# Kernel optimization log

Hardware: AMD Instinct MI355X
Metric: run time of the kernel (lower is better)

Reference implementation:

```python
import jax, jax.numpy as jnp
import numpy as np

B, N, D_IN, D, H_HEADS, DH, M_LAND, ITERS, NCLS = 2, 16384, 1024, 512, 8, 64, 256, 6, 2


def layer_norm(x, g, b, eps=1e-5):
    mu = x.mean(-1, keepdims=True)
    var = ((x - mu) ** 2).mean(-1, keepdims=True)
    return (x - mu) * jax.lax.rsqrt(var + eps) * g + b


def pinv_iter(x, iters):
    # Moore-Penrose pseudo-inverse via Newton-Schulz style iteration (lucidrains nystrom-attention)
    col = jnp.abs(x).sum(-1)
    row = jnp.abs(x).sum(-2)
    z = jnp.swapaxes(x, -1, -2) / (jnp.max(col) * jnp.max(row))
    I = jnp.eye(x.shape[-1], dtype=x.dtype)
    for _ in range(iters):
        xz = x @ z
        z = 0.25 * z @ (13.0 * I - xz @ (15.0 * I - xz @ (7.0 * I - xz)))
    return z


def depthwise_conv(x, w, pad_h, pad_w):
    # x: [B,C,H,W], w: [C,1,kh,kw], groups=C
    return jax.lax.conv_general_dilated(
        x, w, (1, 1), ((pad_h, pad_h), (pad_w, pad_w)),
        dimension_numbers=('NCHW', 'OIHW', 'NCHW'), feature_group_count=x.shape[1])


def nystrom_attention(x, w_qkv, w_out, b_out, res_w):
    b, n, _ = x.shape
    pad = (-n) % M_LAND
    xp = jnp.pad(x, ((0, 0), (pad, 0), (0, 0)))  # pad at front
    npad = n + pad
    qkv = xp @ w_qkv                              # [b, npad, 3D]
    q, k, v = jnp.split(qkv, 3, axis=-1)
    split_heads = lambda t: t.reshape(b, npad, H_HEADS, DH).transpose(0, 2, 1, 3)
    q = split_heads(q) * (DH ** -0.5)
    k = split_heads(k)
    v = split_heads(v)
    l = npad // M_LAND
    # landmarks: mean over contiguous groups '(m l) d -> m d'
    ql = q.reshape(b, H_HEADS, M_LAND, l, DH).mean(3)
    kl = k.reshape(b, H_HEADS, M_LAND, l, DH).mean(3)
    sim1 = jnp.einsum('bhnd,bhmd->bhnm', q, kl)   # [b,h,npad,m]
    sim2 = jnp.einsum('bhid,bhjd->bhij', ql, kl)  # [b,h,m,m]
    sim3 = jnp.einsum('bhmd,bhnd->bhmn', ql, k)   # [b,h,m,npad]
    a1 = jax.nn.softmax(sim1, -1)
    a2 = jax.nn.softmax(sim2, -1)
    a3 = jax.nn.softmax(sim3, -1)
    a2inv = pinv_iter(a2, ITERS)
    out = (a1 @ a2inv) @ (a3 @ v)                 # [b,h,npad,dh]
    # residual depthwise conv over sequence dim, kernel (33,1), per head
    out = out + depthwise_conv(v, res_w, 16, 0)
    out = out.transpose(0, 2, 1, 3).reshape(b, npad, D)
    out = out @ w_out + b_out                     # dropout is identity in eval
    return out[:, -n:]


def ppeg(x, Hs, Ws, w7, b7, w5, b5, w3, b3):
    Bx, _, C = x.shape
    cls_tok, feat = x[:, :1], x[:, 1:]
    f = feat.transpose(0, 2, 1).reshape(Bx, C, Hs, Ws)
    y = (f
         + depthwise_conv(f, w7, 3, 3) + b7[None, :, None, None]
         + depthwise_conv(f, w5, 2, 2) + b5[None, :, None, None]
         + depthwise_conv(f, w3, 1, 1) + b3[None, :, None, None])
    y = y.reshape(Bx, C, Hs * Ws).transpose(0, 2, 1)
    return jnp.concatenate([cls_tok, y], axis=1)


def _forward(x, w_feat, b_feat, cls_token, ln1_g, ln1_b, qkv1, out1_w, out1_b, res1_w,
             ppeg_w7, ppeg_b7, ppeg_w5, ppeg_b5, ppeg_w3, ppeg_b3,
             ln2_g, ln2_b, qkv2, out2_w, out2_b, res2_w, lnf_g, lnf_b, cls_w, cls_b):
    h = jax.nn.gelu(x @ w_feat + b_feat)          # feature embed (dropout off)
    n = h.shape[1]
    side = int(np.ceil(np.sqrt(n)))
    add = side * side - n
    h = jnp.concatenate([h, h[:, :add]], axis=1)  # pad bag to square
    cls = jnp.broadcast_to(cls_token, (h.shape[0], 1, D))
    h = jnp.concatenate([cls, h], axis=1)
    h = h + nystrom_attention(layer_norm(h, ln1_g, ln1_b), qkv1, out1_w, out1_b, res1_w)
    h = ppeg(h, side, side, ppeg_w7, ppeg_b7, ppeg_w5, ppeg_b5, ppeg_w3, ppeg_b3)
    h = h + nystrom_attention(layer_norm(h, ln2_g, ln2_b), qkv2, out2_w, out2_b, res2_w)
    feat0 = layer_norm(h, lnf_g, lnf_b)[:, 0]
    return feat0 @ cls_w + cls_b                  # logits [B, n_classes]


def setup_inputs() -> dict:
    key = jax.random.key(0)
    ks = jax.random.split(key, 16)
    s = jnp.float32(0.02)
    return {
        'x': jax.random.normal(ks[0], (B, N, D_IN), jnp.float32),
        'w_feat': jax.random.normal(ks[1], (D_IN, D), jnp.float32) * s,
        'b_feat': jnp.zeros((D,), jnp.float32),
        'cls_token': jax.random.normal(ks[2], (1, 1, D), jnp.float32) * jnp.float32(1e-6),
        'ln1_g': jnp.ones((D,), jnp.float32), 'ln1_b': jnp.zeros((D,), jnp.float32),
        'qkv1': jax.random.normal(ks[3], (D, 3 * D), jnp.float32) * s,
        'out1_w': jax.random.normal(ks[4], (D, D), jnp.float32) * s,
        'out1_b': jnp.zeros((D,), jnp.float32),
        'res1_w': jax.random.normal(ks[5], (H_HEADS, 1, 33, 1), jnp.float32) * s,
        'ppeg_w7': jax.random.normal(ks[6], (D, 1, 7, 7), jnp.float32) * s,
        'ppeg_b7': jnp.zeros((D,), jnp.float32),
        'ppeg_w5': jax.random.normal(ks[7], (D, 1, 5, 5), jnp.float32) * s,
        'ppeg_b5': jnp.zeros((D,), jnp.float32),
        'ppeg_w3': jax.random.normal(ks[8], (D, 1, 3, 3), jnp.float32) * s,
        'ppeg_b3': jnp.zeros((D,), jnp.float32),
        'ln2_g': jnp.ones((D,), jnp.float32), 'ln2_b': jnp.zeros((D,), jnp.float32),
        'qkv2': jax.random.normal(ks[9], (D, 3 * D), jnp.float32) * s,
        'out2_w': jax.random.normal(ks[10], (D, D), jnp.float32) * s,
        'out2_b': jnp.zeros((D,), jnp.float32),
        'res2_w': jax.random.normal(ks[11], (H_HEADS, 1, 33, 1), jnp.float32) * s,
        'lnf_g': jnp.ones((D,), jnp.float32), 'lnf_b': jnp.zeros((D,), jnp.float32),
        'cls_w': jax.random.normal(ks[12], (D, NCLS), jnp.float32) * s,
        'cls_b': jnp.zeros((NCLS,), jnp.float32),
    }


def reference(x, w_feat, b_feat, cls_token, ln1_g, ln1_b, qkv1, out1_w, out1_b, res1_w,
              ppeg_w7, ppeg_b7, ppeg_w5, ppeg_b5, ppeg_w3, ppeg_b3,
              ln2_g, ln2_b, qkv2, out2_w, out2_b, res2_w, lnf_g, lnf_b, cls_w, cls_b):
    return _forward(x, w_feat, b_feat, cls_token, ln1_g, ln1_b, qkv1, out1_w, out1_b, res1_w,
                    ppeg_w7, ppeg_b7, ppeg_w5, ppeg_b5, ppeg_w3, ppeg_b3,
                    ln2_g, ln2_b, qkv2, out2_w, out2_b, res2_w, lnf_g, lnf_b, cls_w, cls_b)
```

## Files before the change

kernel.cpp:

```cpp
#include <hip/hip_runtime.h>
#include <cstdint>
#include <cstddef>

#define BB 2
#define TT 16385
#define NPAD 16640
#define DD 512
#define HH 8
#define DHH 64
#define MLAND 256
#define PADF 255
#define A3KC 26
#define A3CH 640

typedef __attribute__((ext_vector_type(8))) _Float16 f16x8;
typedef __attribute__((ext_vector_type(4))) float f32x4;

__device__ __forceinline__ float gelu_f(float v) {
  float c = 0.7978845608028654f * (v + 0.044715f * v * v * v);
  return 0.5f * v * (1.0f + tanhf(c));
}

__device__ __forceinline__ unsigned short f16_1(float a) {
  _Float16 h = (_Float16)a;
  return __builtin_bit_cast(unsigned short, h);
}
__device__ __forceinline__ float f16f(unsigned u) {
  return (float)__builtin_bit_cast(_Float16, (unsigned short)(u & 0xffffu));
}
__device__ __forceinline__ unsigned pk_f16(float a, float b) {
  return (unsigned)f16_1(a) | ((unsigned)f16_1(b) << 16);
}
__device__ __forceinline__ void split2h(float a, float b, unsigned& hi, unsigned& lo) {
  _Float16 ah = (_Float16)a, bh = (_Float16)b;
  hi = (unsigned)__builtin_bit_cast(unsigned short, ah) |
       ((unsigned)__builtin_bit_cast(unsigned short, bh) << 16);
  lo = pk_f16(a - (float)ah, b - (float)bh);
}
__device__ __forceinline__ void store4h(float4 v, unsigned short* dh,
                                        unsigned short* dl) {
  unsigned h0, l0, h1, l1;
  split2h(v.x, v.y, h0, l0);
  split2h(v.z, v.w, h1, l1);
  *(uint2*)dh = make_uint2(h0, h1);
  *(uint2*)dl = make_uint2(l0, l1);
}

__device__ __forceinline__ void gload16(const unsigned short* g, short* l) {
  __builtin_amdgcn_global_load_lds(
      (const __attribute__((address_space(1))) void*)g,
      (__attribute__((address_space(3))) void*)l, 16, 0, 0);
}

__global__ void k_set_cls(float* __restrict__ h, const float* __restrict__ cls) {
  h[(size_t)blockIdx.x * TT * DD + threadIdx.x] = cls[threadIdx.x];
}
__global__ void k_copy_cls(float* __restrict__ dst, const float* __restrict__ src) {
  size_t o = (size_t)blockIdx.x * TT * DD + threadIdx.x;
  dst[o] = src[o];
}

__global__ __launch_bounds__(256) void k_cvt_wt(
    const float* __restrict__ W, unsigned short* __restrict__ Wth, int K, int N) {
  __shared__ float tile[32][33];
  int kb = blockIdx.x * 32, nb = blockIdx.y * 32;
  int t = threadIdx.x;
  int tr = t >> 3, tc4 = (t & 7) * 4;
  float4 v = *(const float4*)(W + (size_t)(kb + tr) * N + nb + tc4);
  tile[tr][tc4 + 0] = v.x;
  tile[tr][tc4 + 1] = v.y;
  tile[tr][tc4 + 2] = v.z;
  tile[tr][tc4 + 3] = v.w;
  __syncthreads();
  int n = nb + tr;
  ushort4 hs;
  hs.x = f16_1(tile[tc4 + 0][tr]);
  hs.y = f16_1(tile[tc4 + 1][tr]);
  hs.z = f16_1(tile[tc4 + 2][tr]);
  hs.w = f16_1(tile[tc4 + 3][tr]);
  *(ushort4*)(Wth + (size_t)n * K + kb + tc4) = hs;
}

template <int MODE>
__global__ __launch_bounds__(512) void k_gemm_mfma(
    const float* __restrict__ A, const unsigned short* __restrict__ Aph,
    const unsigned short* __restrict__ Apl, const unsigned short* __restrict__ Wth,
    const float* __restrict__ bias, void* __restrict__ Cv, int M, int K, int N,
    int lda) {
  __shared__ short Ash[128][44];
  __shared__ short Asl[128][44];
  __shared__ short Bsh[256][44];
  const int t = threadIdx.x;
  int nRow = gridDim.x, nCol = gridDim.y;
  int lin = blockIdx.x + blockIdx.y * nRow;
  int chunk = 8 * nCol;
  int group = lin / chunk;
  int rem = lin - group * chunk;
  int gbase = group * 8;
  int Geff = nRow - gbase;
  if (Geff > 8) Geff = 8;
  const int rb = (gbase + rem % Geff) * 128;
  const int cb = (rem / Geff) * 256;
  const float* Ab = A;
  float* Cf = (float*)Cv;
  unsigned short* Ch = (unsigned short*)Cv;
  if (MODE == 2) {
    int b = blockIdx.z;
    Ab = A + (size_t)b * NPAD * DD + (size_t)PADF * DD;
    Cf = (float*)Cv + (size_t)b * TT * DD;
  }
  const int lane = t & 63, wv = t >> 6;
  const int wr = wv >> 2, wc = wv & 3;
  const int fr = lane & 15, kg = lane >> 4;
  const int srow = t >> 2, skh = (t & 3) * 8;
  const int brow = t >> 1, bkh = (t & 1) * 16;

  f32x4 acc[4][4];
  f32x4 zero4 = {0.f, 0.f, 0.f, 0.f};
#pragma unroll
  for (int i = 0; i < 4; ++i)
#pragma unroll
    for (int j = 0; j < 4; ++j) acc[i][j] = zero4;

  for (int k0 = 0; k0 < K; k0 += 32) {
    __syncthreads();
    if (MODE == 1) {
      const unsigned short* ph = Aph + (size_t)(rb + srow) * lda + k0 + skh;
      const unsigned short* pl = Apl + (size_t)(rb + srow) * lda + k0 + skh;
      *(uint4*)&Ash[srow][skh] = *(const uint4*)ph;
      *(uint4*)&Asl[srow][skh] = *(const uint4*)pl;
    } else {
      int grow = rb + srow;
      float4 f0 = {0, 0, 0, 0}, f1 = {0, 0, 0, 0};
      if (grow < M) {
        const float* p = Ab + (size_t)grow * lda + k0 + skh;
        f0 = *(const float4*)p;
        f1 = *(const float4*)(p + 4);
      }
      unsigned h0, h1, h2, h3, l0, l1, l2, l3;
      split2h(f0.x, f0.y, h0, l0);
      split2h(f0.z, f0.w, h1, l1);
      split2h(f1.x, f1.y, h2, l2);
      split2h(f1.z, f1.w, h3, l3);
      *(uint4*)&Ash[srow][skh] = make_uint4(h0, h1, h2, h3);
      *(uint4*)&Asl[srow][skh] = make_uint4(l0, l1, l2, l3);
    }
    {
      const unsigned short* ph = Wth + (size_t)(cb + brow) * K + k0 + bkh;
      *(uint4*)&Bsh[brow][bkh] = *(const uint4*)ph;
      *(uint4*)&Bsh[brow][bkh + 8] = *(const uint4*)(ph + 8);
    }
    __syncthreads();
    f16x8 ah[4], al[4];
#pragma unroll
    for (int mf = 0; mf < 4; ++mf) {
      ah[mf] = *(const f16x8*)&Ash[wr * 64 + mf * 16 + fr][kg * 8];
      al[mf] = *(const f16x8*)&Asl[wr * 64 + mf * 16 + fr][kg * 8];
    }
#pragma unroll
    for (int nf = 0; nf < 4; ++nf) {
      f16x8 bhf = *(const f16x8*)&Bsh[wc * 64 + nf * 16 + fr][kg * 8];
#pragma unroll
      for (int mf = 0; mf < 4; ++mf) {
        acc[mf][nf] =
            __builtin_amdgcn_mfma_f32_16x16x32_f16(ah[mf], bhf, acc[mf][nf], 0, 0, 0);
        acc[mf][nf] =
            __builtin_amdgcn_mfma_f32_16x16x32_f16(al[mf], bhf, acc[mf][nf], 0, 0, 0);
      }
    }
  }
#pragma unroll
  for (int mf = 0; mf < 4; ++mf) {
#pragma unroll
    for (int r = 0; r < 4; ++r) {
      int row = rb + wr * 64 + mf * 16 + kg * 4 + r;
      if (MODE == 2 && row >= M) continue;
      size_t orow = (MODE == 0) ? (size_t)(row + (row >> 14) + 1) : (size_t)row;
#pragma unroll
      for (int nf = 0; nf < 4; ++nf) {
        int col = cb + wc * 64 + nf * 16 + fr;
        float v = acc[mf][nf][r];
        if (MODE == 0) {
          Cf[orow * DD + col] = gelu_f(v + bias[col]);
        } else if (MODE == 1) {
          Ch[orow * (size_t)N + col] = f16_1(v);
        } else {
          float old = Cf[orow * DD + col];
          Cf[orow * DD + col] = old + v + bias[col];
        }
      }
    }
  }
}

__global__ __launch_bounds__(512) void k_gemm_qkv8(
    const unsigned short* __restrict__ Aph, const unsigned short* __restrict__ Apl,
    const unsigned short* __restrict__ Wth, unsigned short* __restrict__ Ch) {
  __shared__ __align__(16) short Ah[2][128][32];
  __shared__ __align__(16) short Al[2][128][32];
  __shared__ __align__(16) short Bs[2][256][32];
  const int t = threadIdx.x;
  int nRow = gridDim.x, nCol = gridDim.y;
  int lin = blockIdx.x + blockIdx.y * nRow;
  int chunk = 8 * nCol;
  int group = lin / chunk;
  int rem = lin - group * chunk;
  int gbase = group * 8;
  int Geff = nRow - gbase;
  if (Geff > 8) Geff = 8;
  const int rb = (gbase + rem % Geff) * 128;
  const int cb = (rem / Geff) * 256;
  const int lane = t & 63, wv = t >> 6;
  const int wr = wv >> 2, wc = wv & 3;
  const int fr = lane & 15, kg = lane >> 4;
  const int lr4 = lane >> 2;
  const int ss = (lane & 3) ^ (lr4 & 3);

  f32x4 acc[4][4];
  f32x4 zero4 = {0.f, 0.f, 0.f, 0.f};
#pragma unroll
  for (int i = 0; i < 4; ++i)
#pragma unroll
    for (int j = 0; j < 4; ++j) acc[i][j] = zero4;

  auto STAGE = [&](int kt, int bf) {
    const int k0 = kt * 32;
    {
      int lr = wv * 16;
      gload16(Aph + (size_t)(rb + lr + lr4) * DD + k0 + ss * 8, &Ah[bf][lr][0]);
      gload16(Apl + (size_t)(rb + lr + lr4) * DD + k0 + ss * 8, &Al[bf][lr][0]);
    }
#pragma unroll
    for (int j = 0; j < 2; ++j) {
      int lr = wv * 32 + j * 16;
      gload16(Wth + (size_t)(cb + lr + lr4) * DD + k0 + ss * 8, &Bs[bf][lr][0]);
    }
  };

  STAGE(0, 0);
  STAGE(1, 1);
  const int sl = ((kg ^ (fr & 3))) * 8;
  for (int kt = 0; kt < 16; ++kt) {
    if (kt < 15) {
      asm volatile("s_waitcnt vmcnt(4)" ::: "memory");
    } else {
      asm volatile("s_waitcnt vmcnt(0)" ::: "memory");
    }
    __builtin_amdgcn_sched_barrier(0);
    __builtin_amdgcn_s_barrier();
    const int bf = kt & 1;
    f16x8 ah[4], al[4];
#pragma unroll
    for (int mf = 0; mf < 4; ++mf) {
      ah[mf] = *(const f16x8*)&Ah[bf][wr * 64 + mf * 16 + fr][sl];
      al[mf] = *(const f16x8*)&Al[bf][wr * 64 + mf * 16 + fr][sl];
    }
#pragma unroll
    for (int nf = 0; nf < 4; ++nf) {
      f16x8 bhf = *(const f16x8*)&Bs[bf][wc * 64 + nf * 16 + fr][sl];
#pragma unroll
      for (int mf = 0; mf < 4; ++mf) {
        acc[mf][nf] =
            __builtin_amdgcn_mfma_f32_16x16x32_f16(ah[mf], bhf, acc[mf][nf], 0, 0, 0);
        acc[mf][nf] =
            __builtin_amdgcn_mfma_f32_16x16x32_f16(al[mf], bhf, acc[mf][nf], 0, 0, 0);
      }
    }
    __builtin_amdgcn_s_barrier();
    if (kt + 2 < 16) STAGE(kt + 2, bf);
  }
#pragma unroll
  for (int mf = 0; mf < 4; ++mf) {
#pragma unroll
    for (int r = 0; r < 4; ++r) {
      int row = rb + wr * 64 + mf * 16 + kg * 4 + r;
#pragma unroll
      for (int nf = 0; nf < 4; ++nf) {
        int col = cb + wc * 64 + nf * 16 + fr;
        Ch[(size_t)row * 1536 + col] = f16_1(acc[mf][nf][r]);
      }
    }
  }
}

__global__ __launch_bounds__(256) void k_ln_pad(
    unsigned short* __restrict__ xph, unsigned short* __restrict__ xpl,
    const float* __restrict__ h, const float* __restrict__ gam,
    const float* __restrict__ bet) {
  int w = threadIdx.x >> 6, lane = threadIdx.x & 63;
  int row = blockIdx.x * 4 + w;
  if (row >= BB * TT) return;
  int b = row / TT, i = row - b * TT;
  const float* src = h + (size_t)row * DD;
  float4 x0 = *(const float4*)(src + lane * 4);
  float4 x1 = *(const float4*)(src + 256 + lane * 4);
  float s = x0.x + x0.y + x0.z + x0.w + x1.x + x1.y + x1.z + x1.w;
  for (int o = 32; o; o >>= 1) s += __shfl_xor(s, o);
  float mu = s * (1.f / 512.f);
  float q = (x0.x - mu) * (x0.x - mu) + (x0.y - mu) * (x0.y - mu) +
            (x0.z - mu) * (x0.z - mu) + (x0.w - mu) * (x0.w - mu) +
            (x1.x - mu) * (x1.x - mu) + (x1.y - mu) * (x1.y - mu) +
            (x1.z - mu) * (x1.z - mu) + (x1.w - mu) * (x1.w - mu);
  for (int o = 32; o; o >>= 1) q += __shfl_xor(q, o);
  float rs = rsqrtf(q * (1.f / 512.f) + 1e-5f);
  float4 g0 = *(const float4*)(gam + lane * 4);
  float4 g1 = *(const float4*)(gam + 256 + lane * 4);
  float4 b0 = *(const float4*)(bet + lane * 4);
  float4 b1 = *(const float4*)(bet + 256 + lane * 4);
  float4 o0, o1;
  o0.x = (x0.x - mu) * rs * g0.x + b0.x;
  o0.y = (x0.y - mu) * rs * g0.y + b0.y;
  o0.z = (x0.z - mu) * rs * g0.z + b0.z;
  o0.w = (x0.w - mu) * rs * g0.w + b0.w;
  o1.x = (x1.x - mu) * rs * g1.x + b1.x;
  o1.y = (x1.y - mu) * rs * g1.y + b1.y;
  o1.z = (x1.z - mu) * rs * g1.z + b1.z;
  o1.w = (x1.w - mu) * rs * g1.w + b1.w;
  size_t ro = ((size_t)b * NPAD + PADF + i) * DD;
  store4h(o0, xph + ro + lane * 4, xpl + ro + lane * 4);
  store4h(o1, xph + ro + 256 + lane * 4, xpl + ro + 256 + lane * 4);
}

__global__ void k_zero_pad(unsigned short* __restrict__ xph,
                           unsigned short* __restrict__ xpl) {
  int r = blockIdx.x;
  int b = r / PADF, j = r - b * PADF;
  size_t ro = ((size_t)b * NPAD + j) * DD;
  ((unsigned*)(xph + ro))[threadIdx.x] = 0u;
  ((unsigned*)(xpl + ro))[threadIdx.x] = 0u;
}

__global__ __launch_bounds__(256) void k_landmarks(
    float* __restrict__ ql, float* __restrict__ kl,
    const unsigned short* __restrict__ qkv) {
  int t = threadIdx.x;
  int mi = t >> 6, d = t & 63;
  int blk = blockIdx.x;
  int bh = blk >> 6, mg = blk & 63;
  int b = bh >> 3, h = bh & 7;
  int m = mg * 4 + mi;
  const unsigned short* base = qkv + (size_t)b * NPAD * 1536 + h * 64 + d;
  float sq = 0.f, sk = 0.f;
  int t0 = m * 65;
  for (int j = 0; j < 65; ++j) {
    const unsigned short* p = base + (size_t)(t0 + j) * 1536;
    sq += f16f(p[0]);
    sk += f16f(p[512]);
  }
  ql[((size_t)bh * 256 + m) * 64 + d] = sq * (0.125f / 65.f);
  kl[((size_t)bh * 256 + m) * 64 + d] = sk * (1.f / 65.f);
}

__global__ __launch_bounds__(256) void k_sim2(
    float* __restrict__ sim, const float* __restrict__ ql, const float* __restrict__ kl) {
  __shared__ __align__(16) float Aq[64][68];
  __shared__ __align__(16) float Bk[64][68];
  int t = threadIdx.x;
  int tj = blockIdx.x, ti = blockIdx.y, bh = blockIdx.z;
  int r = t >> 2, cc = (t & 3) * 16;
  const float* ap = ql + ((size_t)bh * 256 + ti * 64 + r) * 64 + cc;
  const float* bp = kl + ((size_t)bh * 256 + tj * 64 + r) * 64 + cc;
#pragma unroll
  for (int i = 0; i < 16; i += 4) {
    *(float4*)&Aq[r][cc + i] = *(const float4*)(ap + i);
    *(float4*)&Bk[r][cc + i] = *(const float4*)(bp + i);
  }
  __syncthreads();
  int tx = t & 15, ty = t >> 4;
  float acc[4][4];
#pragma unroll
  for (int i = 0; i < 4; ++i)
#pragma unroll
    for (int j = 0; j < 4; ++j) acc[i][j] = 0.f;
  for (int d = 0; d < 64; d += 4) {
    float4 a4[4], b4[4];
#pragma unroll
    for (int ii = 0; ii < 4; ++ii) a4[ii] = *(float4*)&Aq[ty * 4 + ii][d];
#pragma unroll
    for (int jj = 0; jj < 4; ++jj) b4[jj] = *(float4*)&Bk[tx * 4 + jj][d];
#pragma unroll
    for (int ii = 0; ii < 4; ++ii)
#pragma unroll
      for (int jj = 0; jj < 4; ++jj)
        acc[ii][jj] += a4[ii].x * b4[jj].x + a4[ii].y * b4[jj].y + a4[ii].z * b4[jj].z +
                       a4[ii].w * b4[jj].w;
  }
#pragma unroll
  for (int ii = 0; ii < 4; ++ii)
#pragma unroll
    for (int jj = 0; jj < 4; ++jj)
      sim[((size_t)bh * 256 + ti * 64 + ty * 4 + ii) * 256 + tj * 64 + tx * 4 + jj] =
          acc[ii][jj];
}

__global__ __launch_bounds__(256) void k_softmax256(float* __restrict__ a) {
  int w = threadIdx.x >> 6, lane = threadIdx.x & 63;
  size_t row = (size_t)blockIdx.x * 4 + w;
  float* p = a + row * 256 + lane * 4;
  float4 v = *(float4*)p;
  float m = fmaxf(fmaxf(v.x, v.y), fmaxf(v.z, v.w));
  for (int o = 32; o; o >>= 1) m = fmaxf(m, __shfl_xor(m, o));
  v.x = expf(v.x - m); v.y = expf(v.y - m);
  v.z = expf(v.z - m); v.w = expf(v.w - m);
  float s = v.x + v.y + v.z + v.w;
  for (int o = 32; o; o >>= 1) s += __shfl_xor(s, o);
  float inv = 1.f / s;
  v.x *= inv; v.y *= inv; v.z *= inv; v.w *= inv;
  *(float4*)p = v;
}

__global__ void k_pinv_sums(float* __restrict__ red, const float* __restrict__ a2) {
  int bh = blockIdx.x, t = threadIdx.x;
  const float* Ab = a2 + (size_t)bh * 65536;
  float s = 0.f;
  for (int i = 0; i < 256; ++i) s += fabsf(Ab[(size_t)i * 256 + t]);
  red[bh * 256 + t] = s;
  float c = 0.f;
  const float* rp = Ab + (size_t)t * 256;
  for (int j = 0; j < 256; j += 4) {
    float4 v = *(const float4*)(rp + j);
    c += fabsf(v.x) + fabsf(v.y) + fabsf(v.z) + fabsf(v.w);
  }
  red[4096 + bh * 256 + t] = c;
}

__global__ void k_pinv_scale(float* __restrict__ red) {
  __shared__ float sm[8];
  int t = threadIdx.x;
  float m1 = 0.f, m2 = 0.f;
  for (int k = t; k < 4096; k += 256) {
    m1 = fmaxf(m1, red[k]);
    m2 = fmaxf(m2, red[4096 + k]);
  }
  for (int o = 32; o; o >>= 1) {
    m1 = fmaxf(m1, __shfl_xor(m1, o));
    m2 = fmaxf(m2, __shfl_xor(m2, o));
  }
  int w = t >> 6;
  if ((t & 63) == 0) { sm[w] = m1; sm[4 + w] = m2; }
  __syncthreads();
  if (t == 0) {
    float a = fmaxf(fmaxf(sm[0], sm[1]), fmaxf(sm[2], sm[3]));
    float b = fmaxf(fmaxf(sm[4], sm[5]), fmaxf(sm[6], sm[7]));
    red[8192] = 1.0f / (a * b);
  }
}

__global__ void k_zinit(float* __restrict__ z, const float* __restrict__ a2,
                        const float* __restrict__ red) {
  float s = red[8192];
  int i = blockIdx.x, bh = blockIdx.y, j = threadIdx.x;
  z[((size_t)bh * 256 + i) * 256 + j] = a2[((size_t)bh * 256 + j) * 256 + i] * s;
}

__device__ __forceinline__ void bmm_core(
    short (*Ash)[136], short (*Asl)[136], short (*Bsh)[136], short (*Bsl)[136],
    const float* __restrict__ Ab, const float* __restrict__ Bb, int i0, int j0, int N,
    int t, f32x4 (&acc)[4]) {
  const int lane = t & 63, w = t >> 6;
  const int fr = lane & 15, kg = lane >> 4;
  const int ar = t >> 2, akseg = (t & 3) * 32;
  for (int k0 = 0; k0 < 256; k0 += 128) {
    __syncthreads();
    {
      const float* p = Ab + (size_t)(i0 + ar) * 256 + k0 + akseg;
#pragma unroll
      for (int q = 0; q < 4; ++q) {
        float4 f0 = *(const float4*)(p + q * 8);
        float4 f1 = *(const float4*)(p + q * 8 + 4);
        unsigned h0, h1, h2, h3, l0, l1, l2, l3;
        split2h(f0.x, f0.y, h0, l0);
        split2h(f0.z, f0.w, h1, l1);
        split2h(f1.x, f1.y, h2, l2);
        split2h(f1.z, f1.w, h3, l3);
        *(uint4*)&Ash[ar][akseg + q * 8] = make_uint4(h0, h1, h2, h3);
        *(uint4*)&Asl[ar][akseg + q * 8] = make_uint4(l0, l1, l2, l3);
      }
    }
    {
#pragma unroll
      for (int pass = 0; pass < 8; ++pass) {
        int kr = pass * 16 + (t >> 4);
        int jseg = (t & 15) * 4;
        const float* p = Bb + (size_t)(k0 + kr) * N + j0 + jseg;
        float4 f = *(const float4*)p;
        float fv[4] = {f.x, f.y, f.z, f.w};
#pragma unroll
        for (int c = 0; c < 4; ++c) {
          _Float16 hh = (_Float16)fv[c];
          float lo = fv[c] - (float)hh;
          Bsh[jseg + c][kr] = (short)__builtin_bit_cast(unsigned short, hh);
          Bsl[jseg + c][kr] = (short)f16_1(lo);
        }
      }
    }
    __syncthreads();
#pragma unroll
    for (int kw = 0; kw < 4; ++kw) {
      f16x8 bhf = *(const f16x8*)&Bsh[w * 16 + fr][kw * 32 + kg * 8];
      f16x8 blf = *(const f16x8*)&Bsl[w * 16 + fr][kw * 32 + kg * 8];
#pragma unroll
      for (int mf = 0; mf < 4; ++mf) {
        f16x8 ah = *(const f16x8*)&Ash[mf * 16 + fr][kw * 32 + kg * 8];
        f16x8 al = *(const f16x8*)&Asl[mf * 16 + fr][kw * 32 + kg * 8];
        acc[mf] = __builtin_amdgcn_mfma_f32_16x16x32_f16(ah, bhf, acc[mf], 0, 0, 0);
        acc[mf] = __builtin_amdgcn_mfma_f32_16x16x32_f16(al, bhf, acc[mf], 0, 0, 0);
        acc[mf] = __builtin_amdgcn_mfma_f32_16x16x32_f16(ah, blf, acc[mf], 0, 0, 0);
      }
    }
  }
}

__global__ __launch_bounds__(256) void k_bmm_poly(
    const float* __restrict__ A, const float* __restrict__ Bm,
    const float* __restrict__ E, float* __restrict__ C, float a1, float d1, float e1,
    int N) {
  __shared__ short Ash[64][136];
  __shared__ short Asl[64][136];
  __shared__ short Bsh[64][136];
  __shared__ short Bsl[64][136];
  const int t = threadIdx.x;
  const int bh = blockIdx.z;
  const int i0 = blockIdx.y * 64, j0 = blockIdx.x * 64;
  const int lane = t & 63, w = t >> 6;
  const int fr = lane & 15, kg = lane >> 4;
  f32x4 acc[4];
  f32x4 zero4 = {0.f, 0.f, 0.f, 0.f};
#pragma unroll
  for (int i = 0; i < 4; ++i) acc[i] = zero4;
  bmm_core(Ash, Asl, Bsh, Bsl, A + (size_t)bh * 65536, Bm + (size_t)bh * 256 * N, i0,
           j0, N, t, acc);
  int j = j0 + w * 16 + fr;
#pragma unroll
  for (int mf = 0; mf < 4; ++mf) {
#pragma unroll
    for (int rr = 0; rr < 4; ++rr) {
      int i = i0 + mf * 16 + kg * 4 + rr;
      float v = acc[mf][rr];
      size_t off = (size_t)bh * 256 * N + (size_t)i * N + j;
      float out = a1 * v + ((i == j) ? d1 : 0.f);
      if (E) out += e1 * E[off];
      C[off] = out;
    }
  }
}

__global__ __launch_bounds__(256) void k_bmm_dual(
    const float* __restrict__ A0, const float* __restrict__ A1,
    const float* __restrict__ Bm, float* __restrict__ C0, float* __restrict__ C1,
    float s) {
  __shared__ short Ash[64][136];
  __shared__ short Asl[64][136];
  __shared__ short Bsh[64][136];
  __shared__ short Bsl[64][136];
  const int t = threadIdx.x;
  const int z = blockIdx.z;
  const int bh = z & 15;
  const int sel = z >> 4;
  const float* A = sel ? A1 : A0;
  float* C = sel ? C1 : C0;
  const int i0 = blockIdx.y * 64, j0 = blockIdx.x * 64;
  const int lane = t & 63, w = t >> 6;
  const int fr = lane & 15, kg = lane >> 4;
  f32x4 acc[4];
  f32x4 zero4 = {0.f, 0.f, 0.f, 0.f};
#pragma unroll
  for (int i = 0; i < 4; ++i) acc[i] = zero4;
  bmm_core(Ash, Asl, Bsh, Bsl, A + (size_t)bh * 65536, Bm + (size_t)bh * 65536, i0, j0,
           256, t, acc);
  int j = j0 + w * 16 + fr;
#pragma unroll
  for (int mf = 0; mf < 4; ++mf) {
#pragma unroll
    for (int rr = 0; rr < 4; ++rr) {
      int i = i0 + mf * 16 + kg * 4 + rr;
      size_t off = (size_t)bh * 65536 + (size_t)i * 256 + j;
      C[off] = s * acc[mf][rr];
    }
  }
}

__global__ __launch_bounds__(256, 2) void k_a3v_mfma(
    float* __restrict__ pacc, float* __restrict__ pL,
    const float* __restrict__ ql, const unsigned short* __restrict__ qkv) {
  __shared__ short Ks[64][72];
  __shared__ short Vt[64][72];
  __shared__ short Ps[4][64][72];
  const int t = threadIdx.x;
  const int bh = blockIdx.x;
  const int kc = blockIdx.y;
  const int b = bh >> 3, h = bh & 7;
  const int lane = t & 63, w = t >> 6;
  const int fr = lane & 15, kg = lane >> 4;

  f16x8 qf[4][2];
#pragma unroll
  for (int nf = 0; nf < 4; ++nf) {
    const float* qp = ql + ((size_t)bh * 256 + w * 64 + nf * 16 + fr) * 64 + kg * 8;
#pragma unroll
    for (int kw = 0; kw < 2; ++kw) {
      float4 a = *(const float4*)(qp + kw * 32);
      float4 c = *(const float4*)(qp + kw * 32 + 4);
      uint4 uu = make_uint4(pk_f16(a.x, a.y), pk_f16(a.z, a.w), pk_f16(c.x, c.y),
                            pk_f16(c.z, c.w));
      qf[nf][kw] = *(f16x8*)&uu;
    }
  }
  f32x4 oacc[4][4];
  f32x4 zero4 = {0.f, 0.f, 0.f, 0.f};
#pragma unroll
  for (int i = 0; i < 4; ++i)
#pragma unroll
    for (int j = 0; j < 4; ++j) oacc[i][j] = zero4;
  float Lp[4] = {0.f, 0.f, 0.f, 0.f};

  const int skey = t >> 2, sd = (t & 3) * 16;
  const unsigned short* kbase = qkv + (size_t)b * NPAD * 1536 + 512 + h * 64 + sd;

  for (int it = 0; it < A3CH / 64; ++it) {
    int nt = kc * A3CH + it * 64;
    __syncthreads();
    {
      const unsigned short* kp = kbase + (size_t)(nt + skey) * 1536;
      *(uint4*)&Ks[skey][sd] = *(const uint4*)kp;
      *(uint4*)&Ks[skey][sd + 8] = *(const uint4*)(kp + 8);
      const unsigned short* vp = kp + 512;
      uint4 v01 = *(const uint4*)vp;
      uint4 v23 = *(const uint4*)(vp + 8);
      Vt[sd + 0][skey] = (short)v01.x;
      Vt[sd + 1][skey] = (short)(v01.x >> 16);
      Vt[sd + 2][skey] = (short)v01.y;
      Vt[sd + 3][skey] = (short)(v01.y >> 16);
      Vt[sd + 4][skey] = (short)v01.z;
      Vt[sd + 5][skey] = (short)(v01.z >> 16);
      Vt[sd + 6][skey] = (short)v01.w;
      Vt[sd + 7][skey] = (short)(v01.w >> 16);
      Vt[sd + 8][skey] = (short)v23.x;
      Vt[sd + 9][skey] = (short)(v23.x >> 16);
      Vt[sd + 10][skey] = (short)v23.y;
      Vt[sd + 11][skey] = (short)(v23.y >> 16);
      Vt[sd + 12][skey] = (short)v23.z;
      Vt[sd + 13][skey] = (short)(v23.z >> 16);
      Vt[sd + 14][skey] = (short)v23.w;
      Vt[sd + 15][skey] = (short)(v23.w >> 16);
    }
    __syncthreads();
    f32x4 sacc[4][4];
#pragma unroll
    for (int i = 0; i < 4; ++i)
#pragma unroll
      for (int j = 0; j < 4; ++j) sacc[i][j] = zero4;
#pragma unroll
    for (int kw = 0; kw < 2; ++kw) {
      f16x8 kf[4];
#pragma unroll
      for (int mf = 0; mf < 4; ++mf)
        kf[mf] = *(const f16x8*)&Ks[mf * 16 + fr][kw * 32 + kg * 8];
#pragma unroll
      for (int mf = 0; mf < 4; ++mf)
#pragma unroll
        for (int nf = 0; nf < 4; ++nf)
          sacc[mf][nf] = __builtin_amdgcn_mfma_f32_16x16x32_f16(kf[mf], qf[nf][kw],
                                                                sacc[mf][nf], 0, 0, 0);
    }
#pragma unroll
    for (int mf = 0; mf < 4; ++mf)
#pragma unroll
      for (int nf = 0; nf < 4; ++nf) {
        f32x4 s = sacc[mf][nf];
        float p0 = __expf(s[0]);
        float p1 = __expf(s[1]);
        float p2 = __expf(s[2]);
        float p3 = __expf(s[3]);
        Lp[nf] += (p0 + p1) + (p2 + p3);
        uint2 pw = make_uint2(pk_f16(p0, p1), pk_f16(p2, p3));
        *(uint2*)&Ps[w][nf * 16 + fr][mf * 16 + kg * 4] = pw;
      }
    __syncthreads();
#pragma unroll
    for (int kw = 0; kw < 2; ++kw) {
      f16x8 vf[4], pf[4];
#pragma unroll
      for (int mf = 0; mf < 4; ++mf)
        vf[mf] = *(const f16x8*)&Vt[mf * 16 + fr][kw * 32 + kg * 8];
#pragma unroll
      for (int nf = 0; nf < 4; ++nf)
        pf[nf] = *(const f16x8*)&Ps[w][nf * 16 + fr][kw * 32 + kg * 8];
#pragma unroll
      for (int mf = 0; mf < 4; ++mf)
#pragma unroll
        for (int nf = 0; nf < 4; ++nf)
          oacc[mf][nf] = __builtin_amdgcn_mfma_f32_16x16x32_f16(vf[mf], pf[nf],
                                                                oacc[mf][nf], 0, 0, 0);
    }
  }
  size_t obase = ((size_t)kc * 16 + bh) * 256;
#pragma unroll
  for (int mf = 0; mf < 4; ++mf)
#pragma unroll
    for (int nf = 0; nf < 4; ++nf) {
      int lm = w * 64 + nf * 16 + fr;
      *(f32x4*)(pacc + (obase + lm) * 64 + mf * 16 + kg * 4) = oacc[mf][nf];
    }
#pragma unroll
  for (int nf = 0; nf < 4; ++nf) {
    Lp[nf] += __shfl_xor(Lp[nf], 16);
    Lp[nf] += __shfl_xor(Lp[nf], 32);
  }
  if (lane < 16) {
#pragma unroll
    for (int nf = 0; nf < 4; ++nf)
      pL[obase + w * 64 + nf * 16 + lane] = Lp[nf];
  }
}

__global__ __launch_bounds__(64) void k_a3v_red(
    float* __restrict__ bv, const float* __restrict__ pacc,
    const float* __restrict__ pL) {
  int row = blockIdx.x;
  int d = threadIdx.x;
  float A = 0.f, L = 0.f;
#pragma unroll
  for (int c = 0; c < A3KC; ++c) {
    size_t pr = (size_t)c * 4096 + row;
    A += pacc[pr * 64 + d];
    L += pL[pr];
  }
  bv[(size_t)row * 64 + d] = A / L;
}

__global__ __launch_bounds__(256, 2) void k_att1(
    float* __restrict__ attout, const unsigned short* __restrict__ qkv,
    const float* __restrict__ kl, const float* __restrict__ w2) {
  __shared__ short KLs[64][72];
  __shared__ short W2t[64][72];
  __shared__ short Ps[4][64][72];
  const int t = threadIdx.x;
  const int tile = blockIdx.x, bh = blockIdx.y;
  const int b = bh >> 3, h = bh & 7;
  const int lane = t & 63, w = t >> 6;
  const int fr = lane & 15, kg = lane >> 4;
  const int n0 = tile * 256;

  f16x8 qf[4][2];
#pragma unroll
  for (int nf = 0; nf < 4; ++nf) {
    const unsigned short* qp =
        qkv + ((size_t)b * NPAD + n0 + w * 64 + nf * 16 + fr) * 1536 + h * 64 + kg * 8;
    qf[nf][0] = *(const f16x8*)qp;
    qf[nf][1] = *(const f16x8*)(qp + 32);
  }
  f32x4 oacc[4][4];
  f32x4 zero4 = {0.f, 0.f, 0.f, 0.f};
#pragma unroll
  for (int i = 0; i < 4; ++i)
#pragma unroll
    for (int j = 0; j < 4; ++j) oacc[i][j] = zero4;
  float Lp[4] = {0.f, 0.f, 0.f, 0.f};

  const int sr = t >> 2, sc = (t & 3) * 16;
  for (int cb = 0; cb < 4; ++cb) {
    __syncthreads();
    {
      const float* kp = kl + ((size_t)bh * 256 + cb * 64 + sr) * 64 + sc;
      float4 k0 = *(const float4*)kp;
      float4 k1 = *(const float4*)(kp + 4);
      float4 k2 = *(const float4*)(kp + 8);
      float4 k3 = *(const float4*)(kp + 12);
      *(uint4*)&KLs[sr][sc] =
          make_uint4(pk_f16(k0.x * 0.125f, k0.y * 0.125f),
                     pk_f16(k0.z * 0.125f, k0.w * 0.125f),
                     pk_f16(k1.x * 0.125f, k1.y * 0.125f),
                     pk_f16(k1.z * 0.125f, k1.w * 0.125f));
      *(uint4*)&KLs[sr][sc + 8] =
          make_uint4(pk_f16(k2.x * 0.125f, k2.y * 0.125f),
                     pk_f16(k2.z * 0.125f, k2.w * 0.125f),
                     pk_f16(k3.x * 0.125f, k3.y * 0.125f),
                     pk_f16(k3.z * 0.125f, k3.w * 0.125f));
      const float* wp = w2 + ((size_t)bh * 256 + cb * 64 + sr) * 64 + sc;
      float4 v0 = *(const float4*)wp;
      float4 v1 = *(const float4*)(wp + 4);
      float4 v2 = *(const float4*)(wp + 8);
      float4 v3 = *(const float4*)(wp + 12);
      W2t[sc + 0][sr] = (short)f16_1(v0.x);
      W2t[sc + 1][sr] = (short)f16_1(v0.y);
      W2t[sc + 2][sr] = (short)f16_1(v0.z);
      W2t[sc + 3][sr] = (short)f16_1(v0.w);
      W2t[sc + 4][sr] = (short)f16_1(v1.x);
      W2t[sc + 5][sr] = (short)f16_1(v1.y);
      W2t[sc + 6][sr] = (short)f16_1(v1.z);
      W2t[sc + 7][sr] = (short)f16_1(v1.w);
      W2t[sc + 8][sr] = (short)f16_1(v2.x);
      W2t[sc + 9][sr] = (short)f16_1(v2.y);
      W2t[sc + 10][sr] = (short)f16_1(v2.z);
      W2t[sc + 11][sr] = (short)f16_1(v2.w);
      W2t[sc + 12][sr] = (short)f16_1(v3.x);
      W2t[sc + 13][sr] = (short)f16_1(v3.y);
      W2t[sc + 14][sr] = (short)f16_1(v3.z);
      W2t[sc + 15][sr] = (short)f16_1(v3.w);
    }
    __syncthreads();
    f32x4 sacc[4][4];
#pragma unroll
    for (int i = 0; i < 4; ++i)
#pragma unroll
      for (int j = 0; j < 4; ++j) sacc[i][j] = zero4;
#pragma unroll
    for (int kw = 0; kw < 2; ++kw) {
      f16x8 kf[4];
#pragma unroll
      for (int mf = 0; mf < 4; ++mf)
        kf[mf] = *(const f16x8*)&KLs[mf * 16 + fr][kw * 32 + kg * 8];
#pragma unroll
      for (int mf = 0; mf < 4; ++mf)
#pragma unroll
        for (int nf = 0; nf < 4; ++nf)
          sacc[mf][nf] = __builtin_amdgcn_mfma_f32_16x16x32_f16(kf[mf], qf[nf][kw],
                                                                sacc[mf][nf], 0, 0, 0);
    }
#pragma unroll
    for (int mf = 0; mf < 4; ++mf)
#pragma unroll
      for (int nf = 0; nf < 4; ++nf) {
        f32x4 s = sacc[mf][nf];
        float p0 = __expf(s[0]);
        float p1 = __expf(s[1]);
        float p2 = __expf(s[2]);
        float p3 = __expf(s[3]);
        Lp[nf] += (p0 + p1) + (p2 + p3);
        uint2 pw = make_uint2(pk_f16(p0, p1), pk_f16(p2, p3));
        *(uint2*)&Ps[w][nf * 16 + fr][mf * 16 + kg * 4] = pw;
      }
    __syncthreads();
#pragma unroll
    for (int kw = 0; kw < 2; ++kw) {
      f16x8 vf[4], pf[4];
#pragma unroll
      for (int mf = 0; mf < 4; ++mf)
        vf[mf] = *(const f16x8*)&W2t[mf * 16 + fr][kw * 32 + kg * 8];
#pragma unroll
      for (int nf = 0; nf < 4; ++nf)
        pf[nf] = *(const f16x8*)&Ps[w][nf * 16 + fr][kw * 32 + kg * 8];
#pragma unroll
      for (int mf = 0; mf < 4; ++mf)
#pragma unroll
        for (int nf = 0; nf < 4; ++nf)
          oacc[mf][nf] = __builtin_amdgcn_mfma_f32_16x16x32_f16(vf[mf], pf[nf],
                                                                oacc[mf][nf], 0, 0, 0);
    }
  }
#pragma unroll
  for (int nf = 0; nf < 4; ++nf) {
    Lp[nf] += __shfl_xor(Lp[nf], 16);
    Lp[nf] += __shfl_xor(Lp[nf], 32);
  }
#pragma unroll
  for (int nf = 0; nf < 4; ++nf) {
    float inv = 1.0f / Lp[nf];
    int tok = n0 + w * 64 + nf * 16 + fr;
#pragma unroll
    for (int mf = 0; mf < 4; ++mf) {
      f32x4 o = oacc[mf][nf];
      o[0] *= inv; o[1] *= inv; o[2] *= inv; o[3] *= inv;
      *(f32x4*)(attout + ((size_t)b * NPAD + tok) * DD + h * 64 + mf * 16 + kg * 4) = o;
    }
  }
}

__global__ __launch_bounds__(256) void k_convres(
    float* __restrict__ attout, const unsigned short* __restrict__ qkv,
    const float* __restrict__ resw) {
  __shared__ float vS[96][68];
  __shared__ float w33[33];
  int t = threadIdx.x;
  int tb = blockIdx.x, bh = blockIdx.y;
  int b = bh >> 3, h = bh & 7;
  int n0 = tb * 64;
  if (t < 33) w33[t] = resw[h * 33 + t];
  int sc = (t & 3) * 16;
#pragma unroll
  for (int pass = 0; pass < 2; ++pass) {
    int r = (t >> 2) + pass * 64;
    if (r < 96) {
      int seq = n0 - 16 + r;
      if (seq >= 0 && seq < NPAD) {
        const unsigned short* p =
            qkv + ((size_t)b * NPAD + seq) * 1536 + 1024 + h * 64 + sc;
        uint4 u0 = *(const uint4*)p;
        uint4 u1 = *(const uint4*)(p + 8);
        vS[r][sc + 0] = f16f(u0.x); vS[r][sc + 1] = f16f(u0.x >> 16);
        vS[r][sc + 2] = f16f(u0.y); vS[r][sc + 3] = f16f(u0.y >> 16);
        vS[r][sc + 4] = f16f(u0.z); vS[r][sc + 5] = f16f(u0.z >> 16);
        vS[r][sc + 6] = f16f(u0.w); vS[r][sc + 7] = f16f(u0.w >> 16);
        vS[r][sc + 8] = f16f(u1.x); vS[r][sc + 9] = f16f(u1.x >> 16);
        vS[r][sc + 10] = f16f(u1.y); vS[r][sc + 11] = f16f(u1.y >> 16);
        vS[r][sc + 12] = f16f(u1.z); vS[r][sc + 13] = f16f(u1.z >> 16);
        vS[r][sc + 14] = f16f(u1.w); vS[r][sc + 15] = f16f(u1.w >> 16);
      } else {
#pragma unroll
        for (int i = 0; i < 16; ++i) vS[r][sc + i] = 0.f;
      }
    }
  }
  __syncthreads();
  int tg = t >> 5;
  int d2 = (t & 31) * 2;
#pragma unroll
  for (int tk = 0; tk < 8; ++tk) {
    int tokL = tg * 8 + tk;
    float ax = 0.f, ay = 0.f;
    for (int k = 0; k < 33; ++k) {
      float2 v = *(float2*)&vS[tokL + k][d2];
      ax += w33[k] * v.x;
      ay += w33[k] * v.y;
    }
    float* dst = attout + ((size_t)b * NPAD + n0 + tokL) * DD + h * 64 + d2;
    float2 o = *(float2*)dst;
    o.x += ax;
    o.y += ay;
    *(float2*)dst = o;
  }
}

__global__ __launch_bounds__(128) void k_ppeg(
    float* __restrict__ hB, const float* __restrict__ hA,
    const float* __restrict__ w7, const float* __restrict__ b7,
    const float* __restrict__ w5, const float* __restrict__ b5,
    const float* __restrict__ w3, const float* __restrict__ b3) {
  __shared__ float cw[49][128];
  int t = threadIdx.x;
  int i = blockIdx.x >> 2;
  int j0 = (blockIdx.x & 3) * 32;
  int cg = blockIdx.y, b = blockIdx.z;
  int c = cg * 128 + t;
#pragma unroll
  for (int k = 0; k < 49; ++k) cw[k][t] = w7[c * 49 + k];
#pragma unroll
  for (int di = 0; di < 5; ++di)
#pragma unroll
    for (int dj = 0; dj < 5; ++dj)
      cw[(di + 1) * 7 + dj + 1][t] += w5[c * 25 + di * 5 + dj];
#pragma unroll
  for (int di = 0; di < 3; ++di)
#pragma unroll
    for (int dj = 0; dj < 3; ++dj)
      cw[(di + 2) * 7 + dj + 2][t] += w3[c * 9 + di * 3 + dj];
  cw[24][t] += 1.0f;
  float bias = b7[c] + b5[c] + b3[c];
  const float* base = hA + (size_t)b * TT * DD + DD + c;
  float* obase = hB + (size_t)b * TT * DD + DD + c;
  float acc[32];
#pragma unroll
  for (int j = 0; j < 32; ++j) acc[j] = bias;
  for (int di = 0; di < 7; ++di) {
    int ii = i + di - 3;
    if ((unsigned)ii >= 128u) continue;
    float win[38];
#pragma unroll
    for (int w = 0; w < 38; ++w) {
      int col = j0 - 3 + w;
      win[w] = ((unsigned)col < 128u) ? base[(size_t)(ii * 128 + col) * DD] : 0.f;
    }
#pragma unroll
    for (int dj = 0; dj < 7; ++dj) {
      float wv = cw[di * 7 + dj][t];
#pragma unroll
      for (int j = 0; j < 32; ++j) acc[j] += win[j + dj] * wv;
    }
  }
#pragma unroll
  for (int j = 0; j < 32; ++j) obase[(size_t)(i * 128 + j0 + j) * DD] = acc[j];
}

__global__ __launch_bounds__(512) void k_final(
    float* __restrict__ out, const float* __restrict__ h,
    const float* __restrict__ g, const float* __restrict__ be,
    const float* __restrict__ cw, const float* __restrict__ cbias) {
  __shared__ float sm[16];
  int t = threadIdx.x;
  for (int b = 0; b < 2; ++b) {
    const float* row = h + (size_t)b * TT * DD;
    float x = row[t];
    float s = x;
    for (int o = 32; o; o >>= 1) s += __shfl_xor(s, o);
    if ((t & 63) == 0) sm[t >> 6] = s;
    __syncthreads();
    float mu = 0.f;
    for (int i = 0; i < 8; ++i) mu += sm[i];
    mu *= (1.f / 512.f);
    __syncthreads();
    float d = x - mu;
    s = d * d;
    for (int o = 32; o; o >>= 1) s += __shfl_xor(s, o);
    if ((t & 63) == 0) sm[t >> 6] = s;
    __syncthreads();
    float var = 0.f;
    for (int i = 0; i < 8; ++i) var += sm[i];
    var *= (1.f / 512.f);
    float rs = rsqrtf(var + 1e-5f);
    __syncthreads();
    float f = d * rs * g[t] + be[t];
    float p0 = f * cw[2 * t], p1 = f * cw[2 * t + 1];
    for (int o = 32; o; o >>= 1) {
      p0 += __shfl_xor(p0, o);
      p1 += __shfl_xor(p1, o);
    }
    if ((t & 63) == 0) {
      sm[t >> 6] = p0;
      sm[8 + (t >> 6)] = p1;
    }
    __syncthreads();
    if (t == 0) {
      float q0 = 0.f, q1 = 0.f;
      for (int i = 0; i < 8; ++i) {
        q0 += sm[i];
        q1 += sm[8 + i];
      }
      out[b * 2 + 0] = q0 + cbias[0];
      out[b * 2 + 1] = q1 + cbias[1];
    }
    __syncthreads();
  }
}

static void run_attn(float* h, const float* lng, const float* lnb,
                     const float* wqkv, const float* wout, const float* bout,
                     const float* resw, float* xp, unsigned short* qkvh, float* ql,
                     float* kl, float* a2, float* z0, float* z1, float* xz, float* xz2,
                     float* yB, float* yC, float* bv, float* w2, float* red,
                     float* Sbuf, unsigned short* wth, hipStream_t stream) {
  unsigned short* xph = (unsigned short*)xp;
  unsigned short* xpl = xph + (size_t)BB * NPAD * DD;
  k_zero_pad<<<BB * PADF, 256, 0, stream>>>(xph, xpl);
  k_ln_pad<<<(BB * TT + 3) / 4, 256, 0, stream>>>(xph, xpl, h, lng, lnb);
  k_cvt_wt<<<dim3(DD / 32, 1536 / 32), 256, 0, stream>>>(wqkv, wth, DD, 1536);
  k_gemm_qkv8<<<dim3(BB * NPAD / 128, 1536 / 256), 512, 0, stream>>>(xph, xpl, wth,
                                                                     qkvh);
  k_landmarks<<<1024, 256, 0, stream>>>(ql, kl, qkvh);
  float* pacc = Sbuf;
  float* pL = Sbuf + (size_t)A3KC * 4096 * 64;
  k_a3v_mfma<<<dim3(16, A3KC), 256, 0, stream>>>(pacc, pL, ql, qkvh);
  k_a3v_red<<<4096, 64, 0, stream>>>(bv, pacc, pL);
  k_sim2<<<dim3(4, 4, 16), 256, 0, stream>>>(a2, ql, kl);
  k_softmax256<<<1024, 256, 0, stream>>>(a2);
  k_pinv_sums<<<16, 256, 0, stream>>>(red, a2);
  k_pinv_scale<<<1, 256, 0, stream>>>(red);
  k_zinit<<<dim3(256, 16), 256, 0, stream>>>(z0, a2, red);
  float* zc = z0;
  float* zn = z1;
  float* P = xz;
  float* Pn = xz2;
  k_bmm_poly<<<dim3(4, 4, 16), 256, 0, stream>>>(a2, zc, nullptr, P, 1.f, 0.f, 0.f, 256);
  for (int it = 0; it < 6; ++it) {
    k_bmm_poly<<<dim3(4, 4, 16), 256, 0, stream>>>(P, P, P, yB, 1.f, 15.f, -7.f, 256);
    k_bmm_poly<<<dim3(4, 4, 16), 256, 0, stream>>>(P, yB, nullptr, yC, -1.f, 13.f, 0.f, 256);
    k_bmm_dual<<<dim3(4, 4, 32), 256, 0, stream>>>(zc, P, yC, zn, Pn, 0.25f);
    float* tmp = zc; zc = zn; zn = tmp;
    tmp = P; P = Pn; Pn = tmp;
  }
  k_bmm_poly<<<dim3(1, 4, 16), 256, 0, stream>>>(zc, bv, nullptr, w2, 1.f, 0.f, 0.f, 64);
  k_att1<<<dim3(NPAD / 256, 16), 256, 0, stream>>>(xp, qkvh, kl, w2);
  k_convres<<<dim3(NPAD / 64, 16), 256, 0, stream>>>(xp, qkvh, resw);
  k_cvt_wt<<<dim3(DD / 32, DD / 32), 256, 0, stream>>>(wout, wth, DD, DD);
  k_gemm_mfma<2><<<dim3(129, 2, BB), 512, 0, stream>>>(xp, nullptr, nullptr, wth, bout,
                                                       h, TT, DD, DD, DD);
}

extern "C" void kernel_launch(void* const* d_in, const int* in_sizes, int n_in,
                              void* d_out, int out_size, void* d_ws, size_t ws_size,
                              hipStream_t stream) {
  const float* x        = (const float*)d_in[0];
  const float* w_feat   = (const float*)d_in[1];
  const float* b_feat   = (const float*)d_in[2];
  const float* cls_tok  = (const float*)d_in[3];
  const float* ln1_g    = (const float*)d_in[4];
  const float* ln1_b    = (const float*)d_in[5];
  const float* qkv1     = (const float*)d_in[6];
  const float* out1_w   = (const float*)d_in[7];
  const float* out1_b   = (const float*)d_in[8];
  const float* res1_w   = (const float*)d_in[9];
  const float* ppeg_w7  = (const float*)d_in[10];
  const float* ppeg_b7  = (const float*)d_in[11];
  const float* ppeg_w5  = (const float*)d_in[12];
  const float* ppeg_b5  = (const float*)d_in[13];
  const float* ppeg_w3  = (const float*)d_in[14];
  const float* ppeg_b3  = (const float*)d_in[15];
  const float* ln2_g    = (const float*)d_in[16];
  const float* ln2_b    = (const float*)d_in[17];
  const float* qkv2     = (const float*)d_in[18];
  const float* out2_w   = (const float*)d_in[19];
  const float* out2_b   = (const float*)d_in[20];
  const float* res2_w   = (const float*)d_in[21];
  const float* lnf_g    = (const float*)d_in[22];
  const float* lnf_b    = (const float*)d_in[23];
  const float* cls_w    = (const float*)d_in[24];
  const float* cls_b    = (const float*)d_in[25];

  float* ws = (float*)d_ws;
  size_t off = 0;
  float* hA  = ws + off; off += (size_t)BB * TT * DD;
  float* hB  = ws + off; off += (size_t)BB * TT * DD;
  float* xp  = ws + off; off += (size_t)BB * NPAD * DD;
  float* qkvf = ws + off; off += (size_t)BB * NPAD * 3 * DD;
  unsigned short* qkvh = (unsigned short*)qkvf;
  float* ql  = ws + off; off += (size_t)BB * HH * 256 * 64;
  float* kl  = ws + off; off += (size_t)BB * HH * 256 * 64;
  float* a2  = ws + off; off += (size_t)16 * 65536;
  float* z0  = ws + off; off += (size_t)16 * 65536;
  float* z1  = ws + off; off += (size_t)16 * 65536;
  float* xz  = ws + off; off += (size_t)16 * 65536;
  float* xz2 = ws + off; off += (size_t)16 * 65536;
  float* yB  = ws + off; off += (size_t)16 * 65536;
  float* yC  = ws + off; off += (size_t)16 * 65536;
  float* bv  = ws + off; off += (size_t)BB * HH * 256 * 64;
  float* w2  = ws + off; off += (size_t)BB * HH * 256 * 64;
  float* red = ws + off; off += 8448;
  unsigned short* wth = (unsigned short*)(ws + off); off += 393216;

  k_set_cls<<<2, 512, 0, stream>>>(hA, cls_tok);
  k_cvt_wt<<<dim3(1024 / 32, DD / 32), 256, 0, stream>>>(w_feat, wth, 1024, DD);
  k_gemm_mfma<0><<<dim3(32768 / 128, DD / 256), 512, 0, stream>>>(
      x, nullptr, nullptr, wth, b_feat, hA, 32768, 1024, DD, 1024);
  run_attn(hA, ln1_g, ln1_b, qkv1, out1_w, out1_b, res1_w, xp, qkvh, ql, kl, a2, z0, z1,
           xz, xz2, yB, yC, bv, w2, red, hB, wth, stream);
  k_copy_cls<<<2, 512, 0, stream>>>(hB, hA);
  k_ppeg<<<dim3(512, 4, 2), 128, 0, stream>>>(hB, hA, ppeg_w7, ppeg_b7, ppeg_w5, ppeg_b5,
                                              ppeg_w3, ppeg_b3);
  run_attn(hB, ln2_g, ln2_b, qkv2, out2_w, out2_b, res2_w, xp, qkvh, ql, kl, a2, z0, z1,
           xz, xz2, yB, yC, bv, w2, red, hA, wth, stream);
  k_final<<<1, 512, 0, stream>>>((float*)d_out, hB, lnf_g, lnf_b, cls_w, cls_b);
}
```

Measured before the change: 1.594 ms.

## Store attention output as split fp16 and reuse pipelined GEMM for out-projection

k_att1 and k_convres now write the attention output as hi/lo fp16 pairs in the padded xph/xpl buffers instead of fp32. The out-projection then runs on a templated copy of the double-buffered QKV GEMM (k_gemm_pipe<2>), which reads the split fp16 A operand directly and adds the bias and residual into h. This is meant to replace the generic fp32-input k_gemm_mfma path with the faster pipelined split-precision kernel. The risks are small rounding differences from the hi/lo representation, an extra read-modify-write of two buffers in convres, and row reads past NPAD in the last tile of the second batch.

After: 1.696 ms. 6.4% more time.

```diff
diff --git a/kernel.cpp b/kernel.cpp
--- a/kernel.cpp
+++ b/kernel.cpp
@@ -193,9 +193,11 @@
   }
 }
 
-__global__ __launch_bounds__(512) void k_gemm_qkv8(
+template <int PM>
+__global__ __launch_bounds__(512) void k_gemm_pipe(
     const unsigned short* __restrict__ Aph, const unsigned short* __restrict__ Apl,
-    const unsigned short* __restrict__ Wth, unsigned short* __restrict__ Ch) {
+    const unsigned short* __restrict__ Wth, void* __restrict__ Cv,
+    const float* __restrict__ bias) {
   __shared__ __align__(16) short Ah[2][128][32];
   __shared__ __align__(16) short Al[2][128][32];
   __shared__ __align__(16) short Bs[2][256][32];
@@ -216,6 +218,9 @@
   const int lr4 = lane >> 2;
   const int ss = (lane & 3) ^ (lr4 & 3);
 
+  size_t arow0 = (size_t)rb;
+  if (PM == 2) arow0 += (size_t)blockIdx.z * NPAD + PADF;
+
   f32x4 acc[4][4];
   f32x4 zero4 = {0.f, 0.f, 0.f, 0.f};
 #pragma unroll
@@ -227,8 +232,8 @@
     const int k0 = kt * 32;
     {
       int lr = wv * 16;
-      gload16(Aph + (size_t)(rb + lr + lr4) * DD + k0 + ss * 8, &Ah[bf][lr][0]);
-      gload16(Apl + (size_t)(rb + lr + lr4) * DD + k0 + ss * 8, &Al[bf][lr][0]);
+      gload16(Aph + (arow0 + lr + lr4) * DD + k0 + ss * 8, &Ah[bf][lr][0]);
+      gload16(Apl + (arow0 + lr + lr4) * DD + k0 + ss * 8, &Al[bf][lr][0]);
     }
 #pragma unroll
     for (int j = 0; j < 2; ++j) {
@@ -269,15 +274,34 @@
     __builtin_amdgcn_s_barrier();
     if (kt + 2 < 16) STAGE(kt + 2, bf);
   }
-#pragma unroll
-  for (int mf = 0; mf < 4; ++mf) {
-#pragma unroll
-    for (int r = 0; r < 4; ++r) {
-      int row = rb + wr * 64 + mf * 16 + kg * 4 + r;
-#pragma unroll
-      for (int nf = 0; nf < 4; ++nf) {
-        int col = cb + wc * 64 + nf * 16 + fr;
-        Ch[(size_t)row * 1536 + col] = f16_1(acc[mf][nf][r]);
+  if (PM == 1) {
+    unsigned short* Ch = (unsigned short*)Cv;
+#pragma unroll
+    for (int mf = 0; mf < 4; ++mf) {
+#pragma unroll
+      for (int r = 0; r < 4; ++r) {
+        int row = rb + wr * 64 + mf * 16 + kg * 4 + r;
+#pragma unroll
+        for (int nf = 0; nf < 4; ++nf) {
+          int col = cb + wc * 64 + nf * 16 + fr;
+          Ch[(size_t)row * 1536 + col] = f16_1(acc[mf][nf][r]);
+        }
+      }
+    }
+  } else {
+    float* Cf = (float*)Cv + (size_t)blockIdx.z * TT * DD;
+#pragma unroll
+    for (int mf = 0; mf < 4; ++mf) {
+#pragma unroll
+      for (int r = 0; r < 4; ++r) {
+        int row = rb + wr * 64 + mf * 16 + kg * 4 + r;
+        if (row >= TT) continue;
+#pragma unroll
+        for (int nf = 0; nf < 4; ++nf) {
+          int col = cb + wc * 64 + nf * 16 + fr;
+          float old = Cf[(size_t)row * DD + col];
+          Cf[(size_t)row * DD + col] = old + acc[mf][nf][r] + bias[col];
+        }
       }
     }
   }
@@ -730,8 +754,9 @@
 }
 
 __global__ __launch_bounds__(256, 2) void k_att1(
-    float* __restrict__ attout, const unsigned short* __restrict__ qkv,
-    const float* __restrict__ kl, const float* __restrict__ w2) {
+    unsigned short* __restrict__ xph, unsigned short* __restrict__ xpl,
+    const unsigned short* __restrict__ qkv, const float* __restrict__ kl,
+    const float* __restrict__ w2) {
   __shared__ short KLs[64][72];
   __shared__ short W2t[64][72];
   __shared__ short Ps[4][64][72];
@@ -861,15 +886,16 @@
 #pragma unroll
     for (int mf = 0; mf < 4; ++mf) {
       f32x4 o = oacc[mf][nf];
-      o[0] *= inv; o[1] *= inv; o[2] *= inv; o[3] *= inv;
-      *(f32x4*)(attout + ((size_t)b * NPAD + tok) * DD + h * 64 + mf * 16 + kg * 4) = o;
+      float4 ov = make_float4(o[0] * inv, o[1] * inv, o[2] * inv, o[3] * inv);
+      size_t ro = ((size_t)b * NPAD + tok) * DD + h * 64 + mf * 16 + kg * 4;
+      store4h(ov, xph + ro, xpl + ro);
     }
   }
 }
 
 __global__ __launch_bounds__(256) void k_convres(
-    float* __restrict__ attout, const unsigned short* __restrict__ qkv,
-    const float* __restrict__ resw) {
+    unsigned short* __restrict__ xph, unsigned short* __restrict__ xpl,
+    const unsigned short* __restrict__ qkv, const float* __restrict__ resw) {
   __shared__ float vS[96][68];
   __shared__ float w33[33];
   int t = threadIdx.x;
@@ -914,11 +940,15 @@
       ax += w33[k] * v.x;
       ay += w33[k] * v.y;
     }
-    float* dst = attout + ((size_t)b * NPAD + n0 + tokL) * DD + h * 64 + d2;
-    float2 o = *(float2*)dst;
-    o.x += ax;
-    o.y += ay;
-    *(float2*)dst = o;
+    size_t off = ((size_t)b * NPAD + n0 + tokL) * DD + h * 64 + d2;
+    unsigned hv = *(unsigned*)(xph + off);
+    unsigned lv = *(unsigned*)(xpl + off);
+    float x0 = f16f(hv) + f16f(lv) + ax;
+    float x1 = f16f(hv >> 16) + f16f(lv >> 16) + ay;
+    unsigned nh, nl;
+    split2h(x0, x1, nh, nl);
+    *(unsigned*)(xph + off) = nh;
+    *(unsigned*)(xpl + off) = nl;
   }
 }
 
@@ -1034,8 +1064,8 @@
   k_zero_pad<<<BB * PADF, 256, 0, stream>>>(xph, xpl);
   k_ln_pad<<<(BB * TT + 3) / 4, 256, 0, stream>>>(xph, xpl, h, lng, lnb);
   k_cvt_wt<<<dim3(DD / 32, 1536 / 32), 256, 0, stream>>>(wqkv, wth, DD, 1536);
-  k_gemm_qkv8<<<dim3(BB * NPAD / 128, 1536 / 256), 512, 0, stream>>>(xph, xpl, wth,
-                                                                     qkvh);
+  k_gemm_pipe<1><<<dim3(BB * NPAD / 128, 1536 / 256), 512, 0, stream>>>(xph, xpl, wth,
+                                                                        qkvh, nullptr);
   k_landmarks<<<1024, 256, 0, stream>>>(ql, kl, qkvh);
   float* pacc = Sbuf;
   float* pL = Sbuf + (size_t)A3KC * 4096 * 64;
@@ -1059,11 +1089,10 @@
     tmp = P; P = Pn; Pn = tmp;
   }
   k_bmm_poly<<<dim3(1, 4, 16), 256, 0, stream>>>(zc, bv, nullptr, w2, 1.f, 0.f, 0.f, 64);
-  k_att1<<<dim3(NPAD / 256, 16), 256, 0, stream>>>(xp, qkvh, kl, w2);
-  k_convres<<<dim3(NPAD / 64, 16), 256, 0, stream>>>(xp, qkvh, resw);
+  k_att1<<<dim3(NPAD / 256, 16), 256, 0, stream>>>(xph, xpl, qkvh, kl, w2);
+  k_convres<<<dim3(NPAD / 64, 16), 256, 0, stream>>>(xph, xpl, qkvh, resw);
   k_cvt_wt<<<dim3(DD / 32, DD / 32), 256, 0, stream>>>(wout, wth, DD, DD);
-  k_gemm_mfma<2><<<dim3(129, 2, BB), 512, 0, stream>>>(xp, nullptr, nullptr, wth, bout,
-                                                       h, TT, DD, DD, DD);
+  k_gemm_pipe<2><<<dim3(129, 2, BB), 512, 0, stream>>>(xph, xpl, wth, h, bout);
 }
 
 extern "C" void kernel_launch(void* const* d_in, const int* in_sizes, int n_in,
```
